# Performance work log

Measured on AMD Instinct MI355X. Metric: run time of the kernel, lower is better.

The kernel has to match this reference:

```python
import math
import jax, jax.numpy as jnp
import numpy as np

NUM_HEADS = 16
HIDDEN = 1024
FILL = -10000000000000.0


def setup_inputs() -> dict:
    key = jax.random.key(0)
    ks = jax.random.split(key, 12)
    B, S, H = 4, 2048, HIDDEN
    scale = 1.0 / math.sqrt(H)
    inp = {
        "query": jax.random.normal(ks[0], (B, S, H), jnp.float32),
        "key": jax.random.normal(ks[1], (B, S, H), jnp.float32),
        "value": jax.random.normal(ks[2], (B, S, H), jnp.float32),
        "mask": jnp.ones((B, S), jnp.float32),
        # torch.nn.Linear weights are [out, in]; y = x @ W.T + b
        "Wq": jax.random.normal(ks[3], (H, H), jnp.float32) * scale,
        "bq": jax.random.normal(ks[4], (H,), jnp.float32) * 0.01,
        "Wk": jax.random.normal(ks[5], (H, H), jnp.float32) * scale,
        "bk": jax.random.normal(ks[6], (H,), jnp.float32) * 0.01,
        "Wv": jax.random.normal(ks[7], (H, H), jnp.float32) * scale,
        "bv": jax.random.normal(ks[8], (H,), jnp.float32) * 0.01,
        "Wo": jax.random.normal(ks[9], (H, H), jnp.float32) * scale,
        "bo": jax.random.normal(ks[10], (H,), jnp.float32) * 0.01,
    }
    return inp


def reference(query, key, value, mask, Wq, bq, Wk, bk, Wv, bv, Wo, bo):
    B, S, H = query.shape
    nh = NUM_HEADS
    dh = H // nh

    def proj(x, W, b):
        # [B,S,H] -> [B,nh,S,dh]
        y = x @ W.T + b
        return y.reshape(B, S, nh, dh).transpose(0, 2, 1, 3)

    q = proj(query, Wq, bq)
    k = proj(key, Wk, bk)
    v = proj(value, Wv, bv)

    # mask_tril=True: combined padding + causal mask [B,1,S,S]
    tril = jnp.tril(jnp.ones((S, S), query.dtype))
    m = jnp.einsum("bs,ls->bls", mask, tril)[:, None]

    scores = jnp.einsum("bhqd,bhkd->bhqk", q, k) / math.sqrt(dh)
    scores = jnp.where(m == 0, jnp.asarray(FILL, scores.dtype), scores)
    probs = jax.nn.softmax(scores, axis=-1)  # dropout p=0 -> identity

    out = jnp.einsum("bhqv,bhvd->bhqd", probs, v)
    out = out.transpose(0, 2, 1, 3).reshape(B, S, H)
    return out @ Wo.T + bo
```

## Files before the change

kernel.cpp:

```cpp
#include <hip/hip_runtime.h>
#include <hip/hip_bf16.h>
#include <math.h>

#define BATCH 4
#define SEQ   2048
#define HID   1024
#define NH    16
#define DH    64
#define MTOT  (BATCH * SEQ)
#define FILLV (-1e13f)

typedef unsigned short ushort_t;
typedef short bf16x8 __attribute__((ext_vector_type(8)));
typedef float f32x4  __attribute__((ext_vector_type(4)));

__device__ __forceinline__ float bf2f(ushort_t u) {
    return __uint_as_float(((unsigned int)u) << 16);
}
__device__ __forceinline__ ushort_t f2bf(float f) {
    union { __hip_bfloat16 h; ushort_t u; } cv;
    cv.h = __float2bfloat16(f);
    return cv.u;
}

__device__ __forceinline__ void gload16(const void* g, void* l) {
    __builtin_amdgcn_global_load_lds(
        (const __attribute__((address_space(1))) unsigned int*)g,
        (__attribute__((address_space(3))) unsigned int*)l, 16, 0, 0);
}

__global__ __launch_bounds__(256) void cast_f32_bf16(
    const float* __restrict__ x, ushort_t* __restrict__ y, int n4)
{
    const int i = blockIdx.x * 256 + threadIdx.x;
    if (i < n4) {
        const float4 v = ((const float4*)x)[i];
        ushort4 o;
        o.x = f2bf(v.x); o.y = f2bf(v.y); o.z = f2bf(v.z); o.w = f2bf(v.w);
        ((ushort4*)y)[i] = o;
    }
}

template <bool OUT_BF16, bool BIAS_ROW>
__global__ __launch_bounds__(256) void gemm_bt_mfma(
    const ushort_t* __restrict__ A,
    const ushort_t* __restrict__ W,
    const float*    __restrict__ bias,
    void* __restrict__ Yv,
    int M, int N, int K)
{
    __shared__ ushort_t As[2][4096];
    __shared__ ushort_t Bs[2][4096];

    const int tid  = threadIdx.x;
    const int lane = tid & 63;
    const int wave = tid >> 6;
    const int wm   = wave & 1;
    const int wn   = wave >> 1;

    const int flat = blockIdx.y * gridDim.x + blockIdx.x;
    const int cpx  = (gridDim.x * gridDim.y) >> 3;
    const int fl2  = (flat & 7) * cpx + (flat >> 3);
    const int bx   = fl2 % gridDim.x;
    const int by   = fl2 / gridDim.x;

    const int m0   = by * 128;
    const int n0   = bx * 128;
    const int lr   = lane & 15;
    const int lk   = (lane >> 4) * 8;

    f32x4 acc[4][4];
#pragma unroll
    for (int i = 0; i < 4; i++)
#pragma unroll
        for (int j = 0; j < 4; j++) acc[i][j] = (f32x4){0.f, 0.f, 0.f, 0.f};

    auto STAGE = [&](int kk, int d) {
        const ushort_t* a = A + (size_t)(m0 + wave * 32 + lr) * K + kk + lk;
        const ushort_t* w = W + (size_t)(n0 + wave * 32 + lr) * K + kk + lk;
        ushort_t* al = &As[d][wave * 1024];
        ushort_t* bl = &Bs[d][wave * 1024];
        gload16(a,                 al);
        gload16(a + (size_t)16 * K, al + 512);
        gload16(w,                 bl);
        gload16(w + (size_t)16 * K, bl + 512);
    };

    const int nk = K >> 5;
    STAGE(0, 0);

    for (int kt = 0; kt < nk; ++kt) {
        const int d = kt & 1;
        if (kt + 1 < nk) {
            STAGE((kt + 1) << 5, d ^ 1);
            asm volatile("s_waitcnt vmcnt(4)" ::: "memory");
        } else {
            asm volatile("s_waitcnt vmcnt(0)" ::: "memory");
        }
        __builtin_amdgcn_s_barrier();
        __builtin_amdgcn_sched_barrier(0);

        bf16x8 af[4], bf[4];
#pragma unroll
        for (int i = 0; i < 4; i++)
            af[i] = *(const bf16x8*)&As[d][(wm * 4 + i) * 512 + lane * 8];
#pragma unroll
        for (int j = 0; j < 4; j++)
            bf[j] = *(const bf16x8*)&Bs[d][(wn * 4 + j) * 512 + lane * 8];
#pragma unroll
        for (int i = 0; i < 4; i++)
#pragma unroll
            for (int j = 0; j < 4; j++)
                acc[i][j] = __builtin_amdgcn_mfma_f32_16x16x32_bf16(
                    af[i], bf[j], acc[i][j], 0, 0, 0);

        __builtin_amdgcn_sched_barrier(0);
        __builtin_amdgcn_s_barrier();
    }

    const int orow = (lane >> 4) * 4;
    const int ocol = lane & 15;

#pragma unroll
    for (int i = 0; i < 4; i++) {
#pragma unroll
        for (int j = 0; j < 4; j++) {
            const int col = n0 + wn * 64 + j * 16 + ocol;
#pragma unroll
            for (int r = 0; r < 4; r++) {
                const int row = m0 + wm * 64 + i * 16 + orow + r;
                const float bvv = BIAS_ROW ? bias[row] : bias[col];
                const float v = acc[i][j][r] + bvv;
                if (OUT_BF16)
                    ((ushort_t*)Yv)[(size_t)row * N + col] = f2bf(v);
                else
                    ((float*)Yv)[(size_t)row * N + col] = v;
            }
        }
    }
}

__global__ __launch_bounds__(256, 2) void attn_mfma(
    const ushort_t* __restrict__ Qp,
    const ushort_t* __restrict__ Kp,
    const ushort_t* __restrict__ Vt,
    const float*    __restrict__ mask,
    ushort_t* __restrict__ Op)
{
    __shared__ ushort_t Kl[2][4096];
    __shared__ ushort_t Vl[2][4096];
    __shared__ ushort_t PlA[4][16 * 72];
    __shared__ ushort_t PlB[4][16 * 72];

    const int tid  = threadIdx.x;
    const int lane = tid & 63;
    const int wave = tid >> 6;
    const int li   = lane & 15;
    const int lq   = lane >> 4;
    const int blk  = blockIdx.x;
    const int xcd = blk & 7;
    const int jj  = blk >> 3;
    const int bh  = xcd * 8 + (jj & 7);
    const int pp  = jj >> 3;
    const int pr  = pp * 4 + wave;
    const int h   = bh & (NH - 1);
    const int b   = bh >> 4;
    const int prow = lq * 4;

    const int q0a = pr * 16;
    const int q0b = (127 - pr) * 16;
    const int qrowA = q0a + li;
    const int qrowB = q0b + li;
    const int jmaxB = 31 - pp;

    const size_t bSEQ = (size_t)b * SEQ;
    const int    hoff = h * DH;

    const int srow = tid >> 3;
    const int scs8 = ((tid & 7) ^ (srow & 7)) * 8;

    const int fr0 = li * 64 + ((lq ^ (li & 7)) * 8);

    ushort_t* pwA = &PlA[wave][0];
    ushort_t* pwB = &PlB[wave][0];

    const float* mbase = mask + bSEQ + prow;

    const size_t qaA = (bSEQ + qrowA) * HID + hoff + lq * 8;
    const size_t qaB = (bSEQ + qrowB) * HID + hoff + lq * 8;
    const bf16x8 qfA0 = *(const bf16x8*)&Qp[qaA];
    const bf16x8 qfA1 = *(const bf16x8*)&Qp[qaA + 32];
    const bf16x8 qfB0 = *(const bf16x8*)&Qp[qaB];
    const bf16x8 qfB1 = *(const bf16x8*)&Qp[qaB + 32];

    f32x4 oaA[4], oaB[4];
#pragma unroll
    for (int nt = 0; nt < 4; nt++) {
        oaA[nt] = (f32x4){0.f, 0.f, 0.f, 0.f};
        oaB[nt] = (f32x4){0.f, 0.f, 0.f, 0.f};
    }
    float mA = -1e30f, lA = 0.f, mB = -1e30f, lB = 0.f;

    auto STAGE = [&](int js, int bs) {
        const size_t k0s = (size_t)js * 64;
        const ushort_t* kg = Kp + (bSEQ + k0s + srow) * HID + hoff + scs8;
        ushort_t* kl = &Kl[bs][wave * 512];
        gload16(kg, kl);
        gload16(kg + (size_t)32 * HID, kl + 2048);
        const ushort_t* vg = Vt + (size_t)(hoff + srow) * MTOT + bSEQ + k0s + scs8;
        ushort_t* vl = &Vl[bs][wave * 512];
        gload16(vg, vl);
        gload16(vg + (size_t)32 * MTOT, vl + 2048);
    };

    STAGE(0, 0);

    for (int j = 0; j <= jmaxB; ++j) {
        const int  k0  = j * 64;
        const int  bs  = j & 1;
        const bool doA = (j <= pp);

        f32x4 mk[4];
#pragma unroll
        for (int nt = 0; nt < 4; nt++)
            mk[nt] = *(const f32x4*)&mbase[k0 + nt * 16];
        __builtin_amdgcn_sched_barrier(0);

        const int jn = (j < jmaxB) ? (j + 1) : jmaxB;
        STAGE(jn, bs ^ 1);

        asm volatile("s_waitcnt vmcnt(8)" ::: "memory");
        __builtin_amdgcn_s_barrier();
        __builtin_amdgcn_sched_barrier(0);

        bf16x8 kf[4][2];
#pragma unroll
        for (int nt = 0; nt < 4; nt++) {
            const int eo = nt * 1024 + fr0;
            kf[nt][0] = *(const bf16x8*)&Kl[bs][eo];
            kf[nt][1] = *(const bf16x8*)&Kl[bs][eo ^ 32];
        }

        f32x4 saA[4], saB[4];
        __builtin_amdgcn_s_setprio(1);
#pragma unroll
        for (int nt = 0; nt < 4; nt++) {
            f32x4 a = (f32x4){0.f, 0.f, 0.f, 0.f};
            a = __builtin_amdgcn_mfma_f32_16x16x32_bf16(kf[nt][0], qfB0, a, 0, 0, 0);
            a = __builtin_amdgcn_mfma_f32_16x16x32_bf16(kf[nt][1], qfB1, a, 0, 0, 0);
            saB[nt] = a;
        }
        if (doA) {
#pragma unroll
            for (int nt = 0; nt < 4; nt++) {
                f32x4 a = (f32x4){0.f, 0.f, 0.f, 0.f};
                a = __builtin_amdgcn_mfma_f32_16x16x32_bf16(kf[nt][0], qfA0, a, 0, 0, 0);
                a = __builtin_amdgcn_mfma_f32_16x16x32_bf16(kf[nt][1], qfA1, a, 0, 0, 0);
                saA[nt] = a;
            }
        }
        __builtin_amdgcn_s_setprio(0);

        float sB[4][4];
#pragma unroll
        for (int nt = 0; nt < 4; nt++)
#pragma unroll
            for (int r = 0; r < 4; r++) {
                const float v = saB[nt][r] * 0.125f;
                sB[nt][r] = (mk[nt][r] == 0.f) ? FILLV : v;
            }
        if (k0 + 63 > q0b) {
#pragma unroll
            for (int nt = 0; nt < 4; nt++)
#pragma unroll
                for (int r = 0; r < 4; r++) {
                    const int kpos = k0 + nt * 16 + prow + r;
                    sB[nt][r] = (kpos > qrowB) ? FILLV : sB[nt][r];
                }
        }
        float pmB = fmaxf(fmaxf(sB[0][0], sB[0][1]), fmaxf(sB[0][2], sB[0][3]));
#pragma unroll
        for (int nt = 1; nt < 4; nt++)
            pmB = fmaxf(pmB, fmaxf(fmaxf(sB[nt][0], sB[nt][1]),
                                   fmaxf(sB[nt][2], sB[nt][3])));
        pmB = fmaxf(pmB, __shfl_xor(pmB, 16));
        pmB = fmaxf(pmB, __shfl_xor(pmB, 32));
        const float mnB = fmaxf(mB, pmB);
        const float alB = __expf(mB - mnB);
        mB = mnB;
        float psB = 0.f;
#pragma unroll
        for (int nt = 0; nt < 4; nt++) {
            const float p0 = __expf(sB[nt][0] - mnB);
            const float p1 = __expf(sB[nt][1] - mnB);
            const float p2 = __expf(sB[nt][2] - mnB);
            const float p3 = __expf(sB[nt][3] - mnB);
            psB += (p0 + p1) + (p2 + p3);
            ushort4 pk;
            pk.x = f2bf(p0); pk.y = f2bf(p1); pk.z = f2bf(p2); pk.w = f2bf(p3);
            *(ushort4*)&pwB[li * 72 + nt * 16 + prow] = pk;
        }
        psB += __shfl_xor(psB, 16);
        psB += __shfl_xor(psB, 32);
        lB = lB * alB + psB;

        float alA = 1.f;
        if (doA) {
            float sA[4][4];
#pragma unroll
            for (int nt = 0; nt < 4; nt++)
#pragma unroll
                for (int r = 0; r < 4; r++) {
                    const float v = saA[nt][r] * 0.125f;
                    sA[nt][r] = (mk[nt][r] == 0.f) ? FILLV : v;
                }
            if (k0 + 63 > q0a) {
#pragma unroll
                for (int nt = 0; nt < 4; nt++)
#pragma unroll
                    for (int r = 0; r < 4; r++) {
                        const int kpos = k0 + nt * 16 + prow + r;
                        sA[nt][r] = (kpos > qrowA) ? FILLV : sA[nt][r];
                    }
            }
            float pmA = fmaxf(fmaxf(sA[0][0], sA[0][1]), fmaxf(sA[0][2], sA[0][3]));
#pragma unroll
            for (int nt = 1; nt < 4; nt++)
                pmA = fmaxf(pmA, fmaxf(fmaxf(sA[nt][0], sA[nt][1]),
                                       fmaxf(sA[nt][2], sA[nt][3])));
            pmA = fmaxf(pmA, __shfl_xor(pmA, 16));
            pmA = fmaxf(pmA, __shfl_xor(pmA, 32));
            const float mnA = fmaxf(mA, pmA);
            alA = __expf(mA - mnA);
            mA = mnA;
            float psA = 0.f;
#pragma unroll
            for (int nt = 0; nt < 4; nt++) {
                const float p0 = __expf(sA[nt][0] - mnA);
                const float p1 = __expf(sA[nt][1] - mnA);
                const float p2 = __expf(sA[nt][2] - mnA);
                const float p3 = __expf(sA[nt][3] - mnA);
                psA += (p0 + p1) + (p2 + p3);
                ushort4 pk;
                pk.x = f2bf(p0); pk.y = f2bf(p1); pk.z = f2bf(p2); pk.w = f2bf(p3);
                *(ushort4*)&pwA[li * 72 + nt * 16 + prow] = pk;
            }
            psA += __shfl_xor(psA, 16);
            psA += __shfl_xor(psA, 32);
            lA = lA * alA + psA;
        }

        const bf16x8 pfB0 = *(const bf16x8*)&pwB[li * 72 + lq * 8];
        const bf16x8 pfB1 = *(const bf16x8*)&pwB[li * 72 + 32 + lq * 8];
        bf16x8 vf[4][2];
#pragma unroll
        for (int nt = 0; nt < 4; nt++) {
            const int eo = nt * 1024 + fr0;
            vf[nt][0] = *(const bf16x8*)&Vl[bs][eo];
            vf[nt][1] = *(const bf16x8*)&Vl[bs][eo ^ 32];
        }

        __builtin_amdgcn_s_setprio(1);
#pragma unroll
        for (int nt = 0; nt < 4; nt++) {
            f32x4 o = oaB[nt];
#pragma unroll
            for (int r = 0; r < 4; r++) o[r] *= alB;
            o = __builtin_amdgcn_mfma_f32_16x16x32_bf16(vf[nt][0], pfB0, o, 0, 0, 0);
            o = __builtin_amdgcn_mfma_f32_16x16x32_bf16(vf[nt][1], pfB1, o, 0, 0, 0);
            oaB[nt] = o;
        }
        __builtin_amdgcn_s_setprio(0);
        if (doA) {
            const bf16x8 pfA0 = *(const bf16x8*)&pwA[li * 72 + lq * 8];
            const bf16x8 pfA1 = *(const bf16x8*)&pwA[li * 72 + 32 + lq * 8];
            __builtin_amdgcn_s_setprio(1);
#pragma unroll
            for (int nt = 0; nt < 4; nt++) {
                f32x4 o = oaA[nt];
#pragma unroll
                for (int r = 0; r < 4; r++) o[r] *= alA;
                o = __builtin_amdgcn_mfma_f32_16x16x32_bf16(vf[nt][0], pfA0, o, 0, 0, 0);
                o = __builtin_amdgcn_mfma_f32_16x16x32_bf16(vf[nt][1], pfA1, o, 0, 0, 0);
                oaA[nt] = o;
            }
            __builtin_amdgcn_s_setprio(0);
        }

        __builtin_amdgcn_sched_barrier(0);
        __builtin_amdgcn_s_barrier();
    }
    asm volatile("s_waitcnt vmcnt(0)" ::: "memory");

    {
        const float linv = 1.f / lB;
        const size_t obase = (bSEQ + qrowB) * HID + hoff + prow;
#pragma unroll
        for (int nt = 0; nt < 4; nt++) {
            ushort4 ov;
            ov.x = f2bf(oaB[nt][0] * linv);
            ov.y = f2bf(oaB[nt][1] * linv);
            ov.z = f2bf(oaB[nt][2] * linv);
            ov.w = f2bf(oaB[nt][3] * linv);
            *(ushort4*)&Op[obase + nt * 16] = ov;
        }
    }
    {
        const float linv = 1.f / lA;
        const size_t obase = (bSEQ + qrowA) * HID + hoff + prow;
#pragma unroll
        for (int nt = 0; nt < 4; nt++) {
            ushort4 ov;
            ov.x = f2bf(oaA[nt][0] * linv);
            ov.y = f2bf(oaA[nt][1] * linv);
            ov.z = f2bf(oaA[nt][2] * linv);
            ov.w = f2bf(oaA[nt][3] * linv);
            *(ushort4*)&Op[obase + nt * 16] = ov;
        }
    }
}

extern "C" void kernel_launch(void* const* d_in, const int* in_sizes, int n_in,
                              void* d_out, int out_size, void* d_ws, size_t ws_size,
                              hipStream_t stream) {
    const float* query = (const float*)d_in[0];
    const float* key   = (const float*)d_in[1];
    const float* value = (const float*)d_in[2];
    const float* mask  = (const float*)d_in[3];
    const float* Wq    = (const float*)d_in[4];
    const float* bq    = (const float*)d_in[5];
    const float* Wk    = (const float*)d_in[6];
    const float* bk    = (const float*)d_in[7];
    const float* Wv    = (const float*)d_in[8];
    const float* bv    = (const float*)d_in[9];
    const float* Wo    = (const float*)d_in[10];
    const float* bo    = (const float*)d_in[11];

    const size_t eA = (size_t)MTOT * HID;
    const size_t eW = (size_t)HID * HID;
    ushort_t* qb  = (ushort_t*)d_ws;
    ushort_t* kb  = qb  + eA;
    ushort_t* vb  = kb  + eA;
    ushort_t* Qp  = vb  + eA;
    ushort_t* Kp  = Qp  + eA;
    ushort_t* Vtb = Kp  + eA;
    ushort_t* Op  = Vtb + eA;
    ushort_t* wqb = Op  + eA;
    ushort_t* wkb = wqb + eW;
    ushort_t* wvb = wkb + eW;
    ushort_t* wob = wvb + eW;

    const int n4a = (int)(eA / 4), n4w = (int)(eW / 4);
    cast_f32_bf16<<<(n4a + 255) / 256, 256, 0, stream>>>(query, qb, n4a);
    cast_f32_bf16<<<(n4a + 255) / 256, 256, 0, stream>>>(key,   kb, n4a);
    cast_f32_bf16<<<(n4a + 255) / 256, 256, 0, stream>>>(value, vb, n4a);
    cast_f32_bf16<<<(n4w + 255) / 256, 256, 0, stream>>>(Wq, wqb, n4w);
    cast_f32_bf16<<<(n4w + 255) / 256, 256, 0, stream>>>(Wk, wkb, n4w);
    cast_f32_bf16<<<(n4w + 255) / 256, 256, 0, stream>>>(Wv, wvb, n4w);
    cast_f32_bf16<<<(n4w + 255) / 256, 256, 0, stream>>>(Wo, wob, n4w);

    dim3 gg(HID / 128, MTOT / 128);
    gemm_bt_mfma<true, false><<<gg, 256, 0, stream>>>(qb, wqb, bq, Qp, MTOT, HID, HID);
    gemm_bt_mfma<true, false><<<gg, 256, 0, stream>>>(kb, wkb, bk, Kp, MTOT, HID, HID);
    dim3 gv(MTOT / 128, HID / 128);
    gemm_bt_mfma<true, true><<<gv, 256, 0, stream>>>(wvb, vb, bv, Vtb, HID, MTOT, HID);

    attn_mfma<<<(BATCH * NH * 64) / 4, 256, 0, stream>>>(Qp, Kp, Vtb, mask, Op);

    gemm_bt_mfma<false, false><<<gg, 256, 0, stream>>>(Op, wob, bo, d_out, MTOT, HID, HID);
}
```

Before: 411.9 us.

## Merge casts and QKV GEMMs into batched launches with 256x128 triple-buffered tiles

Replaces the seven cast launches with two segmented cast kernels and the three projection GEMMs with a single grid-z batched launch. The GEMM now uses 512-thread blocks with 256x128 tiles, a three-stage LDS pipeline that issues loads two steps ahead, one barrier per k-step, and raised MFMA priority. The output GEMM uses the same body. In attention, the prefetch is issued after the barrier and the vmcnt wait moves to the end of each iteration. The aim is to cut launch overhead and improve GEMM latency hiding and data reuse, at the cost of more LDS per block and fewer, larger blocks.

```diff
diff --git a/kernel.cpp b/kernel.cpp
--- a/kernel.cpp
+++ b/kernel.cpp
@@ -9,6 +9,8 @@
 #define DH    64
 #define MTOT  (BATCH * SEQ)
 #define FILLV (-1e13f)
+#define N4A   (MTOT * HID / 4)
+#define N4W   (HID * HID / 4)
 
 typedef unsigned short ushort_t;
 typedef short bf16x8 __attribute__((ext_vector_type(8)));
@@ -29,45 +31,51 @@
         (__attribute__((address_space(3))) unsigned int*)l, 16, 0, 0);
 }
 
-__global__ __launch_bounds__(256) void cast_f32_bf16(
-    const float* __restrict__ x, ushort_t* __restrict__ y, int n4)
+__device__ __forceinline__ ushort4 cvt4(const float4 v) {
+    ushort4 o;
+    o.x = f2bf(v.x); o.y = f2bf(v.y); o.z = f2bf(v.z); o.w = f2bf(v.w);
+    return o;
+}
+
+__global__ __launch_bounds__(256) void cast3_act(
+    const float* __restrict__ s0, const float* __restrict__ s1,
+    const float* __restrict__ s2, ushort_t* __restrict__ dst)
 {
-    const int i = blockIdx.x * 256 + threadIdx.x;
-    if (i < n4) {
-        const float4 v = ((const float4*)x)[i];
-        ushort4 o;
-        o.x = f2bf(v.x); o.y = f2bf(v.y); o.z = f2bf(v.z); o.w = f2bf(v.w);
-        ((ushort4*)y)[i] = o;
-    }
+    const int i   = blockIdx.x * 256 + threadIdx.x;
+    const int seg = i >> 21;
+    const int off = i & (N4A - 1);
+    const float* s = (seg == 0) ? s0 : (seg == 1) ? s1 : s2;
+    ((ushort4*)dst)[i] = cvt4(((const float4*)s)[off]);
+}
+
+__global__ __launch_bounds__(256) void cast4_w(
+    const float* __restrict__ s0, const float* __restrict__ s1,
+    const float* __restrict__ s2, const float* __restrict__ s3,
+    ushort_t* __restrict__ dst)
+{
+    const int i   = blockIdx.x * 256 + threadIdx.x;
+    const int seg = i >> 18;
+    const int off = i & (N4W - 1);
+    const float* s = (seg == 0) ? s0 : (seg == 1) ? s1 : (seg == 2) ? s2 : s3;
+    ((ushort4*)dst)[i] = cvt4(((const float4*)s)[off]);
 }
 
 template <bool OUT_BF16, bool BIAS_ROW>
-__global__ __launch_bounds__(256) void gemm_bt_mfma(
+__device__ __forceinline__ void gemm_body_256x128(
     const ushort_t* __restrict__ A,
     const ushort_t* __restrict__ W,
-    const float*    __restrict__ bias,
+    const float* __restrict__ bias,
     void* __restrict__ Yv,
-    int M, int N, int K)
+    int Nz, int m0, int n0,
+    ushort_t (*Al)[16 * 512], ushort_t (*Bl)[8 * 512])
 {
-    __shared__ ushort_t As[2][4096];
-    __shared__ ushort_t Bs[2][4096];
-
     const int tid  = threadIdx.x;
     const int lane = tid & 63;
     const int wave = tid >> 6;
-    const int wm   = wave & 1;
-    const int wn   = wave >> 1;
-
-    const int flat = blockIdx.y * gridDim.x + blockIdx.x;
-    const int cpx  = (gridDim.x * gridDim.y) >> 3;
-    const int fl2  = (flat & 7) * cpx + (flat >> 3);
-    const int bx   = fl2 % gridDim.x;
-    const int by   = fl2 / gridDim.x;
-
-    const int m0   = by * 128;
-    const int n0   = bx * 128;
-    const int lr   = lane & 15;
-    const int lk   = (lane >> 4) * 8;
+    const int wm   = wave >> 1;
+    const int wn   = wave & 1;
+    const int li   = lane & 15;
+    const int lq8  = (lane >> 4) * 8;
 
     f32x4 acc[4][4];
 #pragma unroll
@@ -75,69 +83,116 @@
 #pragma unroll
         for (int j = 0; j < 4; j++) acc[i][j] = (f32x4){0.f, 0.f, 0.f, 0.f};
 
+    const ushort_t* aS0 = A + (size_t)(m0 + (2 * wave) * 16 + li) * HID + lq8;
+    const ushort_t* aS1 = aS0 + (size_t)16 * HID;
+    const ushort_t* wS  = W + (size_t)(n0 + wave * 16 + li) * HID + lq8;
+
     auto STAGE = [&](int kk, int d) {
-        const ushort_t* a = A + (size_t)(m0 + wave * 32 + lr) * K + kk + lk;
-        const ushort_t* w = W + (size_t)(n0 + wave * 32 + lr) * K + kk + lk;
-        ushort_t* al = &As[d][wave * 1024];
-        ushort_t* bl = &Bs[d][wave * 1024];
-        gload16(a,                 al);
-        gload16(a + (size_t)16 * K, al + 512);
-        gload16(w,                 bl);
-        gload16(w + (size_t)16 * K, bl + 512);
+        gload16(aS0 + kk, &Al[d][(2 * wave) * 512]);
+        gload16(aS1 + kk, &Al[d][(2 * wave + 1) * 512]);
+        gload16(wS + kk,  &Bl[d][wave * 512]);
     };
 
-    const int nk = K >> 5;
+    const int nk = HID >> 5;
     STAGE(0, 0);
+    STAGE(32, 1);
 
     for (int kt = 0; kt < nk; ++kt) {
-        const int d = kt & 1;
+        const int d = kt % 3;
         if (kt + 1 < nk) {
-            STAGE((kt + 1) << 5, d ^ 1);
-            asm volatile("s_waitcnt vmcnt(4)" ::: "memory");
+            asm volatile("s_waitcnt vmcnt(3)" ::: "memory");
         } else {
             asm volatile("s_waitcnt vmcnt(0)" ::: "memory");
         }
         __builtin_amdgcn_s_barrier();
         __builtin_amdgcn_sched_barrier(0);
+        if (kt + 2 < nk) STAGE((kt + 2) << 5, (kt + 2) % 3);
+        __builtin_amdgcn_sched_barrier(0);
 
         bf16x8 af[4], bf[4];
 #pragma unroll
         for (int i = 0; i < 4; i++)
-            af[i] = *(const bf16x8*)&As[d][(wm * 4 + i) * 512 + lane * 8];
+            af[i] = *(const bf16x8*)&Al[d][(wm * 4 + i) * 512 + lane * 8];
 #pragma unroll
         for (int j = 0; j < 4; j++)
-            bf[j] = *(const bf16x8*)&Bs[d][(wn * 4 + j) * 512 + lane * 8];
+            bf[j] = *(const bf16x8*)&Bl[d][(wn * 4 + j) * 512 + lane * 8];
+        __builtin_amdgcn_s_setprio(1);
 #pragma unroll
         for (int i = 0; i < 4; i++)
 #pragma unroll
             for (int j = 0; j < 4; j++)
                 acc[i][j] = __builtin_amdgcn_mfma_f32_16x16x32_bf16(
                     af[i], bf[j], acc[i][j], 0, 0, 0);
-
-        __builtin_amdgcn_sched_barrier(0);
-        __builtin_amdgcn_s_barrier();
+        __builtin_amdgcn_s_setprio(0);
     }
 
     const int orow = (lane >> 4) * 4;
-    const int ocol = lane & 15;
-
 #pragma unroll
     for (int i = 0; i < 4; i++) {
 #pragma unroll
         for (int j = 0; j < 4; j++) {
-            const int col = n0 + wn * 64 + j * 16 + ocol;
+            const int col = n0 + wn * 64 + j * 16 + li;
 #pragma unroll
             for (int r = 0; r < 4; r++) {
                 const int row = m0 + wm * 64 + i * 16 + orow + r;
                 const float bvv = BIAS_ROW ? bias[row] : bias[col];
                 const float v = acc[i][j][r] + bvv;
                 if (OUT_BF16)
-                    ((ushort_t*)Yv)[(size_t)row * N + col] = f2bf(v);
+                    ((ushort_t*)Yv)[(size_t)row * Nz + col] = f2bf(v);
                 else
-                    ((float*)Yv)[(size_t)row * N + col] = v;
+                    ((float*)Yv)[(size_t)row * Nz + col] = v;
             }
         }
     }
+}
+
+__global__ __launch_bounds__(512, 4) void qkv_gemm(
+    const ushort_t* __restrict__ A0, const ushort_t* __restrict__ A1,
+    const ushort_t* __restrict__ A2,
+    const ushort_t* __restrict__ W0, const ushort_t* __restrict__ W1,
+    const ushort_t* __restrict__ W2,
+    const float* __restrict__ b0, const float* __restrict__ b1,
+    const float* __restrict__ b2,
+    ushort_t* __restrict__ Y0, ushort_t* __restrict__ Y1,
+    ushort_t* __restrict__ Y2)
+{
+    __shared__ ushort_t Al[3][16 * 512];
+    __shared__ ushort_t Bl[3][8 * 512];
+
+    const int z = blockIdx.z;
+    const ushort_t* A    = (z == 0) ? A0 : (z == 1) ? A1 : A2;
+    const ushort_t* W    = (z == 0) ? W0 : (z == 1) ? W1 : W2;
+    const float*    bias = (z == 0) ? b0 : (z == 1) ? b1 : b2;
+    ushort_t*       Y    = (z == 0) ? Y0 : (z == 1) ? Y1 : Y2;
+    const int Nz = (z == 2) ? MTOT : HID;
+    const int gx = Nz >> 7;
+
+    const int flat = blockIdx.x;
+    const int fl2  = (flat & 7) * 32 + (flat >> 3);
+    const int bx   = fl2 % gx;
+    const int by   = fl2 / gx;
+
+    if (z == 2)
+        gemm_body_256x128<true, true>(A, W, bias, Y, Nz, by * 256, bx * 128, Al, Bl);
+    else
+        gemm_body_256x128<true, false>(A, W, bias, Y, Nz, by * 256, bx * 128, Al, Bl);
+}
+
+__global__ __launch_bounds__(512, 4) void gemm_o(
+    const ushort_t* __restrict__ A,
+    const ushort_t* __restrict__ W,
+    const float*    __restrict__ bias,
+    float* __restrict__ Yv)
+{
+    __shared__ ushort_t Al[3][16 * 512];
+    __shared__ ushort_t Bl[3][8 * 512];
+
+    const int flat = blockIdx.x;
+    const int fl2  = (flat & 7) * 32 + (flat >> 3);
+    const int bx   = fl2 % 8;
+    const int by   = fl2 / 8;
+
+    gemm_body_256x128<false, false>(A, W, bias, Yv, HID, by * 256, bx * 128, Al, Bl);
 }
 
 __global__ __launch_bounds__(256, 2) void attn_mfma(
@@ -214,6 +269,8 @@
     };
 
     STAGE(0, 0);
+    asm volatile("s_waitcnt vmcnt(0)" ::: "memory");
+    __builtin_amdgcn_s_barrier();
 
     for (int j = 0; j <= jmaxB; ++j) {
         const int  k0  = j * 64;
@@ -226,11 +283,7 @@
             mk[nt] = *(const f32x4*)&mbase[k0 + nt * 16];
         __builtin_amdgcn_sched_barrier(0);
 
-        const int jn = (j < jmaxB) ? (j + 1) : jmaxB;
-        STAGE(jn, bs ^ 1);
-
-        asm volatile("s_waitcnt vmcnt(8)" ::: "memory");
-        __builtin_amdgcn_s_barrier();
+        if (j < jmaxB) STAGE(j + 1, bs ^ 1);
         __builtin_amdgcn_sched_barrier(0);
 
         bf16x8 kf[4][2];
@@ -388,9 +441,9 @@
         }
 
         __builtin_amdgcn_sched_barrier(0);
+        asm volatile("s_waitcnt vmcnt(0)" ::: "memory");
         __builtin_amdgcn_s_barrier();
     }
-    asm volatile("s_waitcnt vmcnt(0)" ::: "memory");
 
     {
         const float linv = 1.f / lB;
@@ -450,22 +503,13 @@
     ushort_t* wvb = wkb + eW;
     ushort_t* wob = wvb + eW;
 
-    const int n4a = (int)(eA / 4), n4w = (int)(eW / 4);
-    cast_f32_bf16<<<(n4a + 255) / 256, 256, 0, stream>>>(query, qb, n4a);
-    cast_f32_bf16<<<(n4a + 255) / 256, 256, 0, stream>>>(key,   kb, n4a);
-    cast_f32_bf16<<<(n4a + 255) / 256, 256, 0, stream>>>(value, vb, n4a);
-    cast_f32_bf16<<<(n4w + 255) / 256, 256, 0, stream>>>(Wq, wqb, n4w);
-    cast_f32_bf16<<<(n4w + 255) / 256, 256, 0, stream>>>(Wk, wkb, n4w);
-    cast_f32_bf16<<<(n4w + 255) / 256, 256, 0, stream>>>(Wv, wvb, n4w);
-    cast_f32_bf16<<<(n4w + 255) / 256, 256, 0, stream>>>(Wo, wob, n4w);
-
-    dim3 gg(HID / 128, MTOT / 128);
-    gemm_bt_mfma<true, false><<<gg, 256, 0, stream>>>(qb, wqb, bq, Qp, MTOT, HID, HID);
-    gemm_bt_mfma<true, false><<<gg, 256, 0, stream>>>(kb, wkb, bk, Kp, MTOT, HID, HID);
-    dim3 gv(MTOT / 128, HID / 128);
-    gemm_bt_mfma<true, true><<<gv, 256, 0, stream>>>(wvb, vb, bv, Vtb, HID, MTOT, HID);
+    cast3_act<<<3 * N4A / 256, 256, 0, stream>>>(query, key, value, qb);
+    cast4_w  <<<4 * N4W / 256, 256, 0, stream>>>(Wq, Wk, Wv, Wo, wqb);
+
+    qkv_gemm<<<dim3(256, 1, 3), 512, 0, stream>>>(
+        qb, kb, wvb, wqb, wkb, vb, bq, bk, bv, Qp, Kp, Vtb);
 
     attn_mfma<<<(BATCH * NH * 64) / 4, 256, 0, stream>>>(Qp, Kp, Vtb, mask, Op);
 
-    gemm_bt_mfma<false, false><<<gg, 256, 0, stream>>>(Op, wob, bo, d_out, MTOT, HID, HID);
-}
+    gemm_o<<<256, 512, 0, stream>>>(Op, wob, bo, (float*)d_out);
+}
```

New measurement: 383.2 us. 1.07x faster.
